# Performance work log

Measured on AMD Instinct MI355X. Metric: run time of the kernel, lower is better.

Reference implementation:

```python
import jax, jax.numpy as jnp
import numpy as np

H, E, L, NH, DH = 1024, 4, 2, 16, 64
B, LP, LS, HF, MAXTOK = 8, 256, 256, 2816, 30
EPS = 1e-5


def setup_inputs() -> dict:
    key = jax.random.key(0)
    ks = jax.random.split(key, 16)
    n = lambda k, sh, s=0.02: jax.random.normal(k, sh, jnp.float32) * s
    return {
        "pose_feat": jax.random.normal(ks[0], (B, LP, H), jnp.float32),
        "scene_feat": jax.random.normal(ks[1], (B, LS, H), jnp.float32),
        # router Mlp: fc1 Linear(H, E), fc2 Linear(E, E) (hidden_features ignored by Mlp)
        "router_fc1_w": n(ks[2], (H, E)), "router_fc1_b": jnp.zeros((E,), jnp.float32),
        "router_fc2_w": n(ks[3], (E, E)), "router_fc2_b": jnp.zeros((E,), jnp.float32),
        # per-expert, per-layer transformer block params, stacked [E, L, ...]
        "attn_norm_w": jnp.ones((E, L, H), jnp.float32),
        "wq_w": n(ks[4], (E, L, H, H)), "wq_b": jnp.zeros((E, L, H), jnp.float32),
        "wk_w": n(ks[5], (E, L, H, H)), "wk_b": jnp.zeros((E, L, H), jnp.float32),
        "wv_w": n(ks[6], (E, L, H, H)), "wv_b": jnp.zeros((E, L, H), jnp.float32),
        "wo_w": n(ks[7], (E, L, H, H)), "wo_b": jnp.zeros((E, L, H), jnp.float32),
        "ffn_norm_w": jnp.ones((E, L, H), jnp.float32),
        "w1_w": n(ks[8], (E, L, H, HF)),
        "w2_w": n(ks[9], (E, L, HF, H)),
        "w3_w": n(ks[10], (E, L, H, HF)),
        # clip_proj2: Linear(H,H) + LayerNorm(H)
        "proj_w": n(ks[11], (H, H)), "proj_b": jnp.zeros((H,), jnp.float32),
        "ln_w": jnp.ones((H,), jnp.float32), "ln_b": jnp.zeros((H,), jnp.float32),
    }


def _rms(x, w):
    # RMSNorm with eps = norm_eps = 1e-5
    return x * jax.lax.rsqrt(jnp.mean(x * x, axis=-1, keepdims=True) + EPS) * w


def _block(x, anw, qw, qb, kw, kb, vw, vb, ow, ob, fnw, w1, w2, w3):
    b, s, _ = x.shape
    xn = _rms(x, anw)
    q = (xn @ qw + qb).reshape(b, s, NH, DH)
    k = (xn @ kw + kb).reshape(b, s, NH, DH)
    v = (xn @ vw + vb).reshape(b, s, NH, DH)
    scores = jnp.einsum("bqhd,bkhd->bhqk", q, k) / (DH ** 0.5)  # non-causal SDPA
    attn = jax.nn.softmax(scores, axis=-1)
    o = jnp.einsum("bhqk,bkhd->bqhd", attn, v).reshape(b, s, NH * DH)
    h = x + o @ ow + ob
    hn = _rms(h, fnw)
    return h + (jax.nn.silu(hn @ w1) * (hn @ w3)) @ w2  # SwiGLU FFN


def _forward(pose_feat, scene_feat, router_fc1_w, router_fc1_b, router_fc2_w, router_fc2_b,
             attn_norm_w, wq_w, wq_b, wk_w, wk_b, wv_w, wv_b, wo_w, wo_b,
             ffn_norm_w, w1_w, w2_w, w3_w, proj_w, proj_b, ln_w, ln_b):
    x = jnp.concatenate((pose_feat, scene_feat), axis=1)  # [B, S, H]
    # router: sigmoid gates normalized to sum to 1 across experts
    r = jax.nn.sigmoid(jax.nn.gelu(x @ router_fc1_w + router_fc1_b, approximate=False) @ router_fc2_w + router_fc2_b)
    r = r / jnp.maximum(jnp.sum(r, axis=-1, keepdims=True), 1e-8)  # [B, S, E]
    keep = min(x.shape[1], MAXTOK)
    combined = jnp.zeros((x.shape[0], keep, H), x.dtype)
    for e in range(E):  # small fixed expert count
        h = x
        for l in range(L):
            h = _block(h, attn_norm_w[e, l], wq_w[e, l], wq_b[e, l], wk_w[e, l], wk_b[e, l],
                       wv_w[e, l], wv_b[e, l], wo_w[e, l], wo_b[e, l],
                       ffn_norm_w[e, l], w1_w[e, l], w2_w[e, l], w3_w[e, l])
        combined = combined + h[:, :keep] * r[:, :keep, e][:, :, None]
    y = combined @ proj_w + proj_b  # clip_proj2 Linear
    mu = jnp.mean(y, axis=-1, keepdims=True)
    var = jnp.var(y, axis=-1, keepdims=True)
    y = (y - mu) * jax.lax.rsqrt(var + EPS) * ln_w + ln_b  # LayerNorm
    return y.reshape(-1, H)


def reference(pose_feat, scene_feat, router_fc1_w, router_fc1_b, router_fc2_w, router_fc2_b,
              attn_norm_w, wq_w, wq_b, wk_w, wk_b, wv_w, wv_b, wo_w, wo_b,
              ffn_norm_w, w1_w, w2_w, w3_w, proj_w, proj_b, ln_w, ln_b):
    return _forward(pose_feat, scene_feat, router_fc1_w, router_fc1_b, router_fc2_w, router_fc2_b,
                    attn_norm_w, wq_w, wq_b, wk_w, wk_b, wv_w, wv_b, wo_w, wo_b,
                    ffn_norm_w, w1_w, w2_w, w3_w, proj_w, proj_b, ln_w, ln_b)
```

## Files before the change

kernel.cpp:

```cpp
#include <hip/hip_runtime.h>
#include <cstdint>
#include <cstddef>

#define HDIM 1024
#define NE 4
#define NL 2
#define NHD 16
#define SEQ 512
#define BATCH 8
#define HFF 2816
#define KEEP 30
#define KEEPT (BATCH*KEEP)
#define TOK (BATCH*SEQ)
#define MKP 256
#define EPSV 1e-5f

typedef __bf16 bf16;
typedef bf16 bf16x8 __attribute__((ext_vector_type(8)));
typedef bf16 bf16x4 __attribute__((ext_vector_type(4)));
typedef float f32x4 __attribute__((ext_vector_type(4)));

__device__ __forceinline__ void gll16(const bf16* g, bf16* l) {
  __builtin_amdgcn_global_load_lds((const __attribute__((address_space(1))) void*)g,
                                   (__attribute__((address_space(3))) void*)l, 16, 0, 0);
}

__global__ __launch_bounds__(256) void k_concat(const float* __restrict__ pose,
                                                const float* __restrict__ scene,
                                                float* __restrict__ x) {
  int idx4 = blockIdx.x * 256 + threadIdx.x;
  int tok = idx4 >> 8;
  int c = (idx4 & 255) << 2;
  int b = tok >> 9, s = tok & 511;
  const float* src = (s < 256) ? (pose + ((size_t)(b*256 + s)*HDIM + c))
                               : (scene + ((size_t)(b*256 + (s-256))*HDIM + c));
  *(f32x4*)(x + (size_t)tok*HDIM + c) = *(const f32x4*)src;
}

__global__ __launch_bounds__(64) void k_router(const float* __restrict__ x,
                                               const float* __restrict__ w1, const float* __restrict__ b1,
                                               const float* __restrict__ w2, const float* __restrict__ b2,
                                               float* __restrict__ r) {
  int row = blockIdx.x;
  int b = row / KEEP, s = row - b*KEEP;
  int lane = threadIdx.x;
  const float* xr = x + (size_t)(b*SEQ + s)*HDIM;
  float p0=0.f, p1=0.f, p2=0.f, p3=0.f;
  for (int k2 = lane; k2 < HDIM; k2 += 64) {
    float xv = xr[k2];
    const float* wr = w1 + k2*4;
    p0 += xv*wr[0]; p1 += xv*wr[1]; p2 += xv*wr[2]; p3 += xv*wr[3];
  }
  #pragma unroll
  for (int off = 32; off; off >>= 1) {
    p0 += __shfl_xor(p0, off); p1 += __shfl_xor(p1, off);
    p2 += __shfl_xor(p2, off); p3 += __shfl_xor(p3, off);
  }
  if (lane == 0) {
    float gg[4] = {p0 + b1[0], p1 + b1[1], p2 + b1[2], p3 + b1[3]};
    #pragma unroll
    for (int i = 0; i < 4; i++) gg[i] = 0.5f*gg[i]*(1.f + erff(gg[i]*0.70710678f));
    float rr[4], sum = 0.f;
    #pragma unroll
    for (int i = 0; i < 4; i++) {
      float a = b2[i];
      #pragma unroll
      for (int j = 0; j < 4; j++) a += gg[j]*w2[j*4 + i];
      rr[i] = 1.f/(1.f + __expf(-a));
      sum += rr[i];
    }
    float inv = 1.f / fmaxf(sum, 1e-8f);
    #pragma unroll
    for (int i = 0; i < 4; i++) r[row*4 + i] = rr[i]*inv;
  }
}

__global__ __launch_bounds__(256) void k_rmsnorm(const float* __restrict__ in,
                                                 const float* __restrict__ w,
                                                 bf16* __restrict__ out) {
  int row = blockIdx.x, tid = threadIdx.x;
  const float* xr = in + (size_t)row*HDIM;
  f32x4 v = *(const f32x4*)(xr + tid*4);
  float ss = v[0]*v[0] + v[1]*v[1] + v[2]*v[2] + v[3]*v[3];
  #pragma unroll
  for (int off = 32; off; off >>= 1) ss += __shfl_xor(ss, off);
  __shared__ float part[4];
  if ((tid & 63) == 0) part[tid >> 6] = ss;
  __syncthreads();
  float scale = rsqrtf((part[0]+part[1]+part[2]+part[3]) * (1.f/HDIM) + EPSV);
  f32x4 wv = *(const f32x4*)(w + tid*4);
  bf16x4 o;
  #pragma unroll
  for (int i = 0; i < 4; i++) o[i] = (bf16)(v[i]*scale*wv[i]);
  *(bf16x4*)(out + (size_t)row*HDIM + tid*4) = o;
}

struct ConvArgs { const float* src[7]; bf16* dst[7]; };
__global__ __launch_bounds__(256) void k_convertT(ConvArgs a) {
  int id = blockIdx.x;
  int t, base;
  if (id < 4096)      { t = id >> 10; base = t << 10; }
  else if (id < 6912) { t = 4; base = 4096; }
  else if (id < 9728) { t = 5; base = 6912; }
  else                { t = 6; base = 9728; }
  int K = (t == 6) ? HFF : HDIM;
  int N = (t == 4 || t == 5) ? HFF : HDIM;
  int tl = id - base;
  int tilesN = N >> 5;
  int tk = tl / tilesN, tn = tl - tk*tilesN;
  __shared__ float tile[32][33];
  int tx = threadIdx.x & 31, ty = threadIdx.x >> 5;
  const float* src = a.src[t];
  bf16* dst = a.dst[t];
  #pragma unroll
  for (int i = 0; i < 4; i++) {
    int rr = ty + i*8;
    tile[rr][tx] = src[(size_t)(tk*32 + rr)*N + tn*32 + tx];
  }
  __syncthreads();
  #pragma unroll
  for (int i = 0; i < 4; i++) {
    int rr = ty + i*8;
    dst[(size_t)(tn*32 + rr)*K + tk*32 + tx] = (bf16)tile[tx][rr];
  }
}

__global__ __launch_bounds__(256) void k_pack_bias(const float* __restrict__ qb, const float* __restrict__ kb,
                                                   const float* __restrict__ vb, float* __restrict__ dst) {
  int idx = blockIdx.x*256 + threadIdx.x;
  int el = idx / 3072, j = idx - el*3072;
  float v = (j < 1024) ? qb[el*1024 + j]
          : (j < 2048) ? kb[el*1024 + j - 1024]
                       : vb[el*1024 + j - 2048];
  dst[idx] = v;
}

__global__ __launch_bounds__(256) void k_gemm(const bf16* __restrict__ A, const bf16* __restrict__ Bt,
    const float* __restrict__ bias, const float* __restrict__ resid, const bf16* __restrict__ siluSrc,
    float* __restrict__ outF, bf16* __restrict__ outB, int N, int K) {
  __shared__ bf16 As[128*32];
  __shared__ bf16 Bs[128*32];
  int tid = threadIdx.x;
  int wave = tid >> 6, lane = tid & 63;
  int quad = lane >> 4, l16 = lane & 15;
  int wm = (wave >> 1) * 64, wn = (wave & 1) * 64;
  int m0 = blockIdx.y * 128, n0 = blockIdx.x * 128;
  f32x4 zero4 = {0.f, 0.f, 0.f, 0.f};
  f32x4 acc[4][4];
  #pragma unroll
  for (int i = 0; i < 4; i++)
    #pragma unroll
    for (int j = 0; j < 4; j++) acc[i][j] = zero4;
  int srow = wave*32 + (lane >> 2);
  int scol = (lane & 3) * 8;
  const bf16* Ap = A + (size_t)(m0 + srow)*K + scol;
  const bf16* Bp = Bt + (size_t)(n0 + srow)*K + scol;
  bf16* AsW = As + wave*1024;
  bf16* BsW = Bs + wave*1024;
  for (int k0 = 0; k0 < K; k0 += 32) {
    __syncthreads();
    gll16(Ap + k0,                AsW);
    gll16(Ap + k0 + (size_t)16*K, AsW + 512);
    gll16(Bp + k0,                BsW);
    gll16(Bp + k0 + (size_t)16*K, BsW + 512);
    __syncthreads();
    bf16x8 af[4], bq[4];
    #pragma unroll
    for (int i = 0; i < 4; i++) af[i] = *(const bf16x8*)&As[(wm + i*16 + l16)*32 + quad*8];
    #pragma unroll
    for (int i = 0; i < 4; i++) bq[i] = *(const bf16x8*)&Bs[(wn + i*16 + l16)*32 + quad*8];
    #pragma unroll
    for (int mi = 0; mi < 4; mi++)
      #pragma unroll
      for (int ni = 0; ni < 4; ni++)
        acc[mi][ni] = __builtin_amdgcn_mfma_f32_16x16x32_bf16(af[mi], bq[ni], acc[mi][ni], 0, 0, 0);
  }
  #pragma unroll
  for (int mi = 0; mi < 4; mi++) {
    #pragma unroll
    for (int ni = 0; ni < 4; ni++) {
      int colg = n0 + wn + ni*16 + l16;
      float bv = bias ? bias[colg] : 0.f;
      #pragma unroll
      for (int rr = 0; rr < 4; rr++) {
        int rowg = m0 + wm + mi*16 + quad*4 + rr;
        size_t off = (size_t)rowg*N + colg;
        float vv = acc[mi][ni][rr] + bv;
        if (resid) vv += resid[off];
        if (siluSrc) { float a = (float)siluSrc[off]; vv *= a / (1.f + __expf(-a)); }
        if (outF) outF[off] = vv;
        else      outB[off] = (bf16)vv;
      }
    }
  }
}

__global__ __launch_bounds__(256) void k_vtrans(const bf16* __restrict__ v, bf16* __restrict__ vt, int vs) {
  __shared__ bf16 t[64][72];
  int b = blockIdx.z, h = blockIdx.y, s0 = blockIdx.x * 64;
  int r = threadIdx.x >> 2, c0 = (threadIdx.x & 3) * 16;
  const bf16* vp = v + (size_t)(b*SEQ + s0 + r)*vs + h*64 + c0;
  bf16x8 v0 = *(const bf16x8*)vp;
  bf16x8 v1 = *(const bf16x8*)(vp + 8);
  #pragma unroll
  for (int j = 0; j < 8; j++) { t[r][c0+j] = v0[j]; t[r][c0+8+j] = v1[j]; }
  __syncthreads();
  bf16x8 o0, o1;
  #pragma unroll
  for (int j = 0; j < 8; j++) { o0[j] = t[c0+j][r]; o1[j] = t[c0+8+j][r]; }
  bf16* op = vt + ((size_t)(b*NHD + h)*64 + r)*512 + s0 + c0;
  *(bf16x8*)op = o0;
  *(bf16x8*)(op + 8) = o1;
}

__global__ __launch_bounds__(256, 1) void k_attn_mfma(const bf16* __restrict__ q,
    const bf16* __restrict__ k, const bf16* __restrict__ vt,
    bf16* __restrict__ o, int qlen, int orb, int qs) {
  __shared__ bf16 Ps[4][16][520];
  int tid = threadIdx.x;
  int wave = tid >> 6, lane = tid & 63;
  int quad = lane >> 4, l16 = lane & 15;
  int b = blockIdx.z, head = blockIdx.y;
  int q0 = blockIdx.x * 64 + wave * 16;

  const bf16* qp = q + (size_t)(b*SEQ + q0 + l16)*qs + head*64 + quad*8;
  bf16x8 aq0 = *(const bf16x8*)(qp);
  bf16x8 aq1 = *(const bf16x8*)(qp + 32);

  f32x4 z = {0.f, 0.f, 0.f, 0.f};
  f32x4 acc[32];
  #pragma unroll
  for (int ni = 0; ni < 32; ni++) acc[ni] = z;
  const bf16* kb = k + (size_t)(b*SEQ + l16)*qs + head*64 + quad*8;
  #pragma unroll
  for (int ni = 0; ni < 32; ni++) {
    const bf16* kp = kb + (size_t)(ni*16)*qs;
    bf16x8 b0 = *(const bf16x8*)(kp);
    bf16x8 b1 = *(const bf16x8*)(kp + 32);
    acc[ni] = __builtin_amdgcn_mfma_f32_16x16x32_bf16(aq0, b0, acc[ni], 0, 0, 0);
    acc[ni] = __builtin_amdgcn_mfma_f32_16x16x32_bf16(aq1, b1, acc[ni], 0, 0, 0);
  }
  float mx[4] = {-3e30f, -3e30f, -3e30f, -3e30f};
  #pragma unroll
  for (int ni = 0; ni < 32; ni++)
    #pragma unroll
    for (int rr = 0; rr < 4; rr++) {
      float s = acc[ni][rr] * 0.125f;
      acc[ni][rr] = s;
      mx[rr] = fmaxf(mx[rr], s);
    }
  #pragma unroll
  for (int off = 1; off <= 8; off <<= 1)
    #pragma unroll
    for (int rr = 0; rr < 4; rr++)
      mx[rr] = fmaxf(mx[rr], __shfl_xor(mx[rr], off));
  float sm[4] = {0.f, 0.f, 0.f, 0.f};
  #pragma unroll
  for (int ni = 0; ni < 32; ni++)
    #pragma unroll
    for (int rr = 0; rr < 4; rr++) {
      float p = __expf(acc[ni][rr] - mx[rr]);
      acc[ni][rr] = p;
      sm[rr] += p;
    }
  #pragma unroll
  for (int off = 1; off <= 8; off <<= 1)
    #pragma unroll
    for (int rr = 0; rr < 4; rr++)
      sm[rr] += __shfl_xor(sm[rr], off);
  #pragma unroll
  for (int ni = 0; ni < 32; ni++)
    #pragma unroll
    for (int rr = 0; rr < 4; rr++)
      Ps[wave][quad*4 + rr][ni*16 + l16] = (bf16)acc[ni][rr];
  const bf16* vtb = vt + ((size_t)(b*NHD + head)*64 + l16)*512 + quad*8;
  f32x4 accO[4] = {z, z, z, z};
  #pragma unroll 4
  for (int kk = 0; kk < 16; kk++) {
    bf16x8 ap = *(const bf16x8*)&Ps[wave][l16][kk*32 + quad*8];
    #pragma unroll
    for (int ni = 0; ni < 4; ni++) {
      bf16x8 bv = *(const bf16x8*)(vtb + (size_t)(ni*16)*512 + kk*32);
      accO[ni] = __builtin_amdgcn_mfma_f32_16x16x32_bf16(ap, bv, accO[ni], 0, 0, 0);
    }
  }
  float inv[4];
  #pragma unroll
  for (int rr = 0; rr < 4; rr++) inv[rr] = 1.f / sm[rr];
  #pragma unroll
  for (int ni = 0; ni < 4; ni++)
    #pragma unroll
    for (int rr = 0; rr < 4; rr++) {
      int row = q0 + quad*4 + rr;
      if (row < qlen)
        o[(size_t)(b*orb + row)*HDIM + head*64 + ni*16 + l16] = (bf16)(accO[ni][rr] * inv[rr]);
    }
}

__global__ __launch_bounds__(256) void k_gather(const float* __restrict__ h,
                                                float* __restrict__ hk, bf16* __restrict__ ok) {
  int idx = blockIdx.x*256 + threadIdx.x;
  int row = idx >> 10, col = idx & 1023;
  if (row < BATCH*KEEP) {
    int b = row / KEEP, s = row - b*KEEP;
    hk[idx] = h[(size_t)(b*SEQ + s)*HDIM + col];
  } else {
    hk[idx] = 0.f;
    ok[idx] = (bf16)0.f;
  }
}

__global__ __launch_bounds__(256) void k_accum(float* __restrict__ comb, const float* __restrict__ hk,
                                               const float* __restrict__ r, int e, int first) {
  int idx = blockIdx.x*256 + threadIdx.x;
  int row = idx >> 10;
  float vv = hk[idx] * r[row*4 + e];
  comb[idx] = (first ? 0.f : comb[idx]) + vv;
}

__global__ __launch_bounds__(256) void k_proj(const float* __restrict__ comb,
                                              const float* __restrict__ pw,
                                              float* __restrict__ part) {
  int rg = blockIdx.x, ks = blockIdx.y, tid = threadIdx.x;
  __shared__ float xr[8][64];
  for (int i = tid; i < 8*64; i += 256) {
    int r = i >> 6, kk = i & 63;
    xr[r][kk] = comb[(size_t)(rg*8 + r)*HDIM + ks*64 + kk];
  }
  __syncthreads();
  f32x4 acc[8];
  #pragma unroll
  for (int r = 0; r < 8; r++) acc[r] = (f32x4){0.f,0.f,0.f,0.f};
  const float* wp = pw + (size_t)(ks*64)*HDIM + tid*4;
  #pragma unroll 4
  for (int kk = 0; kk < 64; kk++) {
    f32x4 w4 = *(const f32x4*)(wp + (size_t)kk*HDIM);
    #pragma unroll
    for (int r = 0; r < 8; r++) acc[r] += xr[r][kk] * w4;
  }
  #pragma unroll
  for (int r = 0; r < 8; r++)
    *(f32x4*)(part + ((size_t)ks*KEEPT + rg*8 + r)*HDIM + tid*4) = acc[r];
}

__global__ __launch_bounds__(256) void k_ln(const float* __restrict__ part, const float* __restrict__ pb,
    const float* __restrict__ lnw, const float* __restrict__ lnb, float* __restrict__ out) {
  int row = blockIdx.x, tid = threadIdx.x;
  f32x4 acc = *(const f32x4*)(pb + tid*4);
  #pragma unroll
  for (int s = 0; s < 16; s++)
    acc += *(const f32x4*)(part + ((size_t)s*KEEPT + row)*HDIM + tid*4);
  float ps = acc[0]+acc[1]+acc[2]+acc[3];
  #pragma unroll
  for (int off = 32; off; off >>= 1) ps += __shfl_xor(ps, off);
  __shared__ float red1[4], red2[4];
  if ((tid & 63) == 0) red1[tid >> 6] = ps;
  __syncthreads();
  float mu = (red1[0]+red1[1]+red1[2]+red1[3]) * (1.f/HDIM);
  f32x4 d;
  #pragma unroll
  for (int i = 0; i < 4; i++) d[i] = acc[i] - mu;
  float pv = d[0]*d[0]+d[1]*d[1]+d[2]*d[2]+d[3]*d[3];
  #pragma unroll
  for (int off = 32; off; off >>= 1) pv += __shfl_xor(pv, off);
  if ((tid & 63) == 0) red2[tid >> 6] = pv;
  __syncthreads();
  float rs = rsqrtf((red2[0]+red2[1]+red2[2]+red2[3]) * (1.f/HDIM) + EPSV);
  f32x4 lw = *(const f32x4*)(lnw + tid*4);
  f32x4 lb = *(const f32x4*)(lnb + tid*4);
  f32x4 o;
  #pragma unroll
  for (int i = 0; i < 4; i++) o[i] = d[i]*rs*lw[i] + lb[i];
  *(f32x4*)(out + (size_t)row*HDIM + tid*4) = o;
}

extern "C" void kernel_launch(void* const* d_in, const int* in_sizes, int n_in,
                              void* d_out, int out_size, void* d_ws, size_t ws_size,
                              hipStream_t stream) {
  (void)in_sizes; (void)n_in; (void)out_size; (void)ws_size;
  const float* pose = (const float*)d_in[0];
  const float* scene = (const float*)d_in[1];
  const float* rf1w = (const float*)d_in[2];
  const float* rf1b = (const float*)d_in[3];
  const float* rf2w = (const float*)d_in[4];
  const float* rf2b = (const float*)d_in[5];
  const float* anw = (const float*)d_in[6];
  const float* wqw = (const float*)d_in[7];
  const float* wqb = (const float*)d_in[8];
  const float* wkw = (const float*)d_in[9];
  const float* wkb = (const float*)d_in[10];
  const float* wvw = (const float*)d_in[11];
  const float* wvb = (const float*)d_in[12];
  const float* wow = (const float*)d_in[13];
  const float* wob = (const float*)d_in[14];
  const float* fnw = (const float*)d_in[15];
  const float* w1w = (const float*)d_in[16];
  const float* w2w = (const float*)d_in[17];
  const float* w3w = (const float*)d_in[18];
  const float* pw  = (const float*)d_in[19];
  const float* pb  = (const float*)d_in[20];
  const float* lnw = (const float*)d_in[21];
  const float* lnb = (const float*)d_in[22];
  float* out = (float*)d_out;

  char* p = (char*)d_ws;
  auto carve = [&](size_t bytes) { void* r = (void*)p; p += (bytes + 255) & ~(size_t)255; return r; };
  float* x   = (float*)carve((size_t)TOK*HDIM*4);
  float* h   = (float*)carve((size_t)TOK*HDIM*4);
  bf16* xn   = (bf16*)carve((size_t)TOK*HDIM*2);
  bf16* qkv3 = (bf16*)carve((size_t)TOK*3072*2);
  bf16* ob_  = (bf16*)carve((size_t)TOK*HDIM*2);
  bf16* vt   = (bf16*)carve((size_t)TOK*HDIM*2);
  bf16* a1   = (bf16*)carve((size_t)TOK*HFF*2);
  bf16* g    = (bf16*)carve((size_t)TOK*HFF*2);
  bf16* qkvT = (bf16*)carve((size_t)3072*HDIM*2);
  bf16* woT  = (bf16*)carve((size_t)HDIM*HDIM*2);
  bf16* w1T  = (bf16*)carve((size_t)HDIM*HFF*2);
  bf16* w3T  = (bf16*)carve((size_t)HDIM*HFF*2);
  bf16* w2T  = (bf16*)carve((size_t)HFF*HDIM*2);
  float* hk  = (float*)carve((size_t)MKP*HDIM*4);
  bf16* hnk  = (bf16*)carve((size_t)MKP*HDIM*2);
  bf16* okb  = (bf16*)carve((size_t)MKP*HDIM*2);
  float* comb = (float*)carve((size_t)KEEPT*HDIM*4);
  float* rbuf = (float*)carve((size_t)KEEPT*4*4);
  float* qkvb = (float*)carve((size_t)8*3072*4);
  float* part = (float*)a1;

  k_concat<<<4096, 256, 0, stream>>>(pose, scene, x);
  k_router<<<KEEPT, 64, 0, stream>>>(x, rf1w, rf1b, rf2w, rf2b, rbuf);
  k_pack_bias<<<96, 256, 0, stream>>>(wqb, wkb, wvb, qkvb);

  for (int e = 0; e < NE; e++) {
    for (int l = 0; l < NL; l++) {
      int el = e*NL + l;
      ConvArgs ca;
      ca.src[0] = wqw + (size_t)el*HDIM*HDIM;
      ca.src[1] = wkw + (size_t)el*HDIM*HDIM;
      ca.src[2] = wvw + (size_t)el*HDIM*HDIM;
      ca.src[3] = wow + (size_t)el*HDIM*HDIM;
      ca.src[4] = w1w + (size_t)el*HDIM*HFF;
      ca.src[5] = w3w + (size_t)el*HDIM*HFF;
      ca.src[6] = w2w + (size_t)el*HFF*HDIM;
      ca.dst[0] = qkvT;
      ca.dst[1] = qkvT + (size_t)1024*HDIM;
      ca.dst[2] = qkvT + (size_t)2048*HDIM;
      ca.dst[3] = woT;
      ca.dst[4] = w1T; ca.dst[5] = w3T; ca.dst[6] = w2T;
      k_convertT<<<12544, 256, 0, stream>>>(ca);

      const float* src_h = (l == 0) ? x : h;
      k_rmsnorm<<<TOK, 256, 0, stream>>>(src_h, anw + (size_t)el*HDIM, xn);
      k_gemm<<<dim3(24, 32), 256, 0, stream>>>(xn, qkvT, qkvb + (size_t)el*3072,
                                               nullptr, nullptr, nullptr, qkv3, 3072, HDIM);
      k_vtrans<<<dim3(8, NHD, BATCH), 256, 0, stream>>>(qkv3 + 2048, vt, 3072);

      if (l == 0) {
        k_attn_mfma<<<dim3(8, NHD, BATCH), 256, 0, stream>>>(qkv3, qkv3 + 1024, vt, ob_, SEQ, SEQ, 3072);
        k_gemm<<<dim3(8, 32), 256, 0, stream>>>(ob_, woT, wob + (size_t)el*HDIM, x, nullptr, h, nullptr, HDIM, HDIM);
        k_rmsnorm<<<TOK, 256, 0, stream>>>(h, fnw + (size_t)el*HDIM, xn);
        k_gemm<<<dim3(22, 32), 256, 0, stream>>>(xn, w1T, nullptr, nullptr, nullptr, nullptr, a1, HFF, HDIM);
        k_gemm<<<dim3(22, 32), 256, 0, stream>>>(xn, w3T, nullptr, nullptr, a1, nullptr, g, HFF, HDIM);
        k_gemm<<<dim3(8, 32), 256, 0, stream>>>(g, w2T, nullptr, h, nullptr, h, nullptr, HDIM, HFF);
      } else {
        k_attn_mfma<<<dim3(1, NHD, BATCH), 256, 0, stream>>>(qkv3, qkv3 + 1024, vt, okb, KEEP, KEEP, 3072);
        k_gather<<<1024, 256, 0, stream>>>(h, hk, okb);
        k_gemm<<<dim3(8, 2), 256, 0, stream>>>(okb, woT, wob + (size_t)el*HDIM, hk, nullptr, hk, nullptr, HDIM, HDIM);
        k_rmsnorm<<<MKP, 256, 0, stream>>>(hk, fnw + (size_t)el*HDIM, hnk);
        k_gemm<<<dim3(22, 2), 256, 0, stream>>>(hnk, w1T, nullptr, nullptr, nullptr, nullptr, a1, HFF, HDIM);
        k_gemm<<<dim3(22, 2), 256, 0, stream>>>(hnk, w3T, nullptr, nullptr, a1, nullptr, g, HFF, HDIM);
        k_gemm<<<dim3(8, 2), 256, 0, stream>>>(g, w2T, nullptr, hk, nullptr, hk, nullptr, HDIM, HFF);
        k_accum<<<960, 256, 0, stream>>>(comb, hk, rbuf, e, (e == 0) ? 1 : 0);
      }
    }
  }
  k_proj<<<dim3(30, 16), 256, 0, stream>>>(comb, pw, part);
  k_ln<<<KEEPT, 256, 0, stream>>>(part, pb, lnw, lnb, out);
}
```

Measured before the change: 3.247 ms.

## Add 256x256 double-buffered GEMM and fuse W1/W3 into one SwiGLU GEMM

Adds a 512-thread GEMM kernel with 256x256 tiles, double-buffered LDS loads and priority-raised MFMA phases, and uses it for the QKV projection and the FFN up-projections. The W1 and W3 weights are interleaved in 16-row groups into one transposed buffer, so a single GEMM computes both and applies SiLU-gating in its epilogue. This removes one GEMM launch, the a1 intermediate write and read, and a second pass over the activations. In exchange it uses larger tiles with fewer blocks, which may limit occupancy for the small 256-row keep path.

Result: faster. 2.872 ms (-11.5%).

```diff
diff --git a/kernel.cpp b/kernel.cpp
--- a/kernel.cpp
+++ b/kernel.cpp
@@ -121,7 +121,12 @@
   #pragma unroll
   for (int i = 0; i < 4; i++) {
     int rr = ty + i*8;
-    dst[(size_t)(tn*32 + rr)*K + tk*32 + tx] = (bf16)tile[tx][rr];
+    int gr = tn*32 + rr;
+    size_t dr;
+    if (t == 4)      dr = (size_t)((gr >> 4)*32 + (gr & 15));
+    else if (t == 5) dr = (size_t)((gr >> 4)*32 + 16 + (gr & 15));
+    else             dr = (size_t)gr;
+    dst[dr*K + tk*32 + tx] = (bf16)tile[tx][rr];
   }
 }
 
@@ -191,6 +196,113 @@
         if (outF) outF[off] = vv;
         else      outB[off] = (bf16)vv;
       }
+    }
+  }
+}
+
+__global__ __launch_bounds__(512, 2) void k_gemm256(const bf16* __restrict__ A, const bf16* __restrict__ Bt,
+    const float* __restrict__ bias, bf16* __restrict__ out, int N, int K, int swiglu) {
+  __shared__ __align__(16) bf16 As[2][256*32];
+  __shared__ __align__(16) bf16 Bs[2][256*32];
+  int tid = threadIdx.x;
+  int wave = tid >> 6, lane = tid & 63;
+  int quad = lane >> 4, l16 = lane & 15;
+  int wm128 = (wave >> 2) * 128;
+  int wn64  = (wave & 3) * 64;
+  int m0 = blockIdx.y * 256, n0 = blockIdx.x * 256;
+  int NT = K >> 5;
+  f32x4 z = {0.f, 0.f, 0.f, 0.f};
+  f32x4 acc[8][4];
+  #pragma unroll
+  for (int i = 0; i < 8; i++)
+    #pragma unroll
+    for (int j = 0; j < 4; j++) acc[i][j] = z;
+  const bf16* aSrc = A + (size_t)(m0 + wave*16 + (lane>>2))*K + (lane&3)*8;
+  const bf16* bSrc = Bt + (size_t)(n0 + wave*16 + (lane>>2))*K + (lane&3)*8;
+  auto stage = [&](int buf, int kt) {
+    #pragma unroll
+    for (int r = 0; r < 2; r++) {
+      gll16(aSrc + (size_t)(r*128)*K + kt*32, &As[buf][(r*128 + wave*16)*32]);
+      gll16(bSrc + (size_t)(r*128)*K + kt*32, &Bs[buf][(r*128 + wave*16)*32]);
+    }
+  };
+  stage(0, 0);
+  stage(1, 1);
+  asm volatile("s_waitcnt vmcnt(4)" ::: "memory");
+  asm volatile("s_barrier" ::: "memory");
+  for (int kt = 0; kt < NT; ++kt) {
+    int cur = kt & 1;
+    bf16x8 pb[4];
+    {
+      bf16x8 pa[4];
+      #pragma unroll
+      for (int i = 0; i < 4; i++)
+        pa[i] = *(const bf16x8*)&As[cur][(wm128 + i*16 + l16)*32 + quad*8];
+      #pragma unroll
+      for (int i = 0; i < 4; i++)
+        pb[i] = *(const bf16x8*)&Bs[cur][(wn64 + i*16 + l16)*32 + quad*8];
+      asm volatile("s_barrier" ::: "memory");
+      __builtin_amdgcn_s_setprio(1);
+      #pragma unroll
+      for (int mi = 0; mi < 4; mi++)
+        #pragma unroll
+        for (int ni = 0; ni < 4; ni++)
+          acc[mi][ni] = __builtin_amdgcn_mfma_f32_16x16x32_bf16(pa[mi], pb[ni], acc[mi][ni], 0, 0, 0);
+      __builtin_amdgcn_s_setprio(0);
+      asm volatile("s_barrier" ::: "memory");
+    }
+    {
+      bf16x8 pa[4];
+      #pragma unroll
+      for (int i = 0; i < 4; i++)
+        pa[i] = *(const bf16x8*)&As[cur][(wm128 + 64 + i*16 + l16)*32 + quad*8];
+      asm volatile("s_barrier" ::: "memory");
+      __builtin_amdgcn_s_setprio(1);
+      #pragma unroll
+      for (int mi = 0; mi < 4; mi++)
+        #pragma unroll
+        for (int ni = 0; ni < 4; ni++)
+          acc[4+mi][ni] = __builtin_amdgcn_mfma_f32_16x16x32_bf16(pa[mi], pb[ni], acc[4+mi][ni], 0, 0, 0);
+      __builtin_amdgcn_s_setprio(0);
+      asm volatile("s_barrier" ::: "memory");
+    }
+    if (kt + 1 < NT) {
+      if (kt + 2 < NT) {
+        stage(cur, kt + 2);
+        asm volatile("s_waitcnt vmcnt(4)" ::: "memory");
+      } else {
+        asm volatile("s_waitcnt vmcnt(0)" ::: "memory");
+      }
+      asm volatile("s_barrier" ::: "memory");
+    }
+  }
+  if (!swiglu) {
+    #pragma unroll
+    for (int ni = 0; ni < 4; ni++) {
+      int colg = n0 + wn64 + ni*16 + l16;
+      float bv = bias ? bias[colg] : 0.f;
+      #pragma unroll
+      for (int mi = 0; mi < 8; mi++)
+        #pragma unroll
+        for (int rr = 0; rr < 4; rr++) {
+          int rowg = m0 + wm128 + mi*16 + quad*4 + rr;
+          out[(size_t)rowg*N + colg] = (bf16)(acc[mi][ni][rr] + bv);
+        }
+    }
+  } else {
+    int half = N >> 1;
+    #pragma unroll
+    for (int np = 0; np < 2; np++) {
+      int colo = ((n0 + wn64) >> 1) + np*16 + l16;
+      #pragma unroll
+      for (int mi = 0; mi < 8; mi++)
+        #pragma unroll
+        for (int rr = 0; rr < 4; rr++) {
+          int rowg = m0 + wm128 + mi*16 + quad*4 + rr;
+          float xv = acc[mi][np*2][rr];
+          float yv = acc[mi][np*2+1][rr];
+          out[(size_t)rowg*half + colo] = (bf16)(xv / (1.f + __expf(-xv)) * yv);
+        }
     }
   }
 }
@@ -415,8 +527,7 @@
   bf16* g    = (bf16*)carve((size_t)TOK*HFF*2);
   bf16* qkvT = (bf16*)carve((size_t)3072*HDIM*2);
   bf16* woT  = (bf16*)carve((size_t)HDIM*HDIM*2);
-  bf16* w1T  = (bf16*)carve((size_t)HDIM*HFF*2);
-  bf16* w3T  = (bf16*)carve((size_t)HDIM*HFF*2);
+  bf16* w13T = (bf16*)carve((size_t)2*HDIM*HFF*2);
   bf16* w2T  = (bf16*)carve((size_t)HFF*HDIM*2);
   float* hk  = (float*)carve((size_t)MKP*HDIM*4);
   bf16* hnk  = (bf16*)carve((size_t)MKP*HDIM*2);
@@ -445,29 +556,26 @@
       ca.dst[1] = qkvT + (size_t)1024*HDIM;
       ca.dst[2] = qkvT + (size_t)2048*HDIM;
       ca.dst[3] = woT;
-      ca.dst[4] = w1T; ca.dst[5] = w3T; ca.dst[6] = w2T;
+      ca.dst[4] = w13T; ca.dst[5] = w13T; ca.dst[6] = w2T;
       k_convertT<<<12544, 256, 0, stream>>>(ca);
 
       const float* src_h = (l == 0) ? x : h;
       k_rmsnorm<<<TOK, 256, 0, stream>>>(src_h, anw + (size_t)el*HDIM, xn);
-      k_gemm<<<dim3(24, 32), 256, 0, stream>>>(xn, qkvT, qkvb + (size_t)el*3072,
-                                               nullptr, nullptr, nullptr, qkv3, 3072, HDIM);
+      k_gemm256<<<dim3(12, 16), 512, 0, stream>>>(xn, qkvT, qkvb + (size_t)el*3072, qkv3, 3072, HDIM, 0);
       k_vtrans<<<dim3(8, NHD, BATCH), 256, 0, stream>>>(qkv3 + 2048, vt, 3072);
 
       if (l == 0) {
         k_attn_mfma<<<dim3(8, NHD, BATCH), 256, 0, stream>>>(qkv3, qkv3 + 1024, vt, ob_, SEQ, SEQ, 3072);
         k_gemm<<<dim3(8, 32), 256, 0, stream>>>(ob_, woT, wob + (size_t)el*HDIM, x, nullptr, h, nullptr, HDIM, HDIM);
         k_rmsnorm<<<TOK, 256, 0, stream>>>(h, fnw + (size_t)el*HDIM, xn);
-        k_gemm<<<dim3(22, 32), 256, 0, stream>>>(xn, w1T, nullptr, nullptr, nullptr, nullptr, a1, HFF, HDIM);
-        k_gemm<<<dim3(22, 32), 256, 0, stream>>>(xn, w3T, nullptr, nullptr, a1, nullptr, g, HFF, HDIM);
+        k_gemm256<<<dim3(22, 16), 512, 0, stream>>>(xn, w13T, nullptr, g, 2*HFF, HDIM, 1);
         k_gemm<<<dim3(8, 32), 256, 0, stream>>>(g, w2T, nullptr, h, nullptr, h, nullptr, HDIM, HFF);
       } else {
         k_attn_mfma<<<dim3(1, NHD, BATCH), 256, 0, stream>>>(qkv3, qkv3 + 1024, vt, okb, KEEP, KEEP, 3072);
         k_gather<<<1024, 256, 0, stream>>>(h, hk, okb);
         k_gemm<<<dim3(8, 2), 256, 0, stream>>>(okb, woT, wob + (size_t)el*HDIM, hk, nullptr, hk, nullptr, HDIM, HDIM);
         k_rmsnorm<<<MKP, 256, 0, stream>>>(hk, fnw + (size_t)el*HDIM, hnk);
-        k_gemm<<<dim3(22, 2), 256, 0, stream>>>(hnk, w1T, nullptr, nullptr, nullptr, nullptr, a1, HFF, HDIM);
-        k_gemm<<<dim3(22, 2), 256, 0, stream>>>(hnk, w3T, nullptr, nullptr, a1, nullptr, g, HFF, HDIM);
+        k_gemm256<<<dim3(22, 1), 512, 0, stream>>>(hnk, w13T, nullptr, g, 2*HFF, HDIM, 1);
         k_gemm<<<dim3(8, 2), 256, 0, stream>>>(g, w2T, nullptr, hk, nullptr, hk, nullptr, HDIM, HFF);
         k_accum<<<960, 256, 0, stream>>>(comb, hk, rbuf, e, (e == 0) ? 1 : 0);
       }
```
